# Performance work log

Measured on AMD Instinct MI355X. Metric: run time of the kernel, lower is better.

## Reference

```python
import jax, jax.numpy as jnp
import numpy as np

DIM_IN = 1024
DIM_OUT = 1024
NUM_HEADS = 16
HEAD_DIM = DIM_OUT // NUM_HEADS


def setup_inputs() -> dict:
    key = jax.random.key(0)
    k1, k2, k3, k4 = jax.random.split(key, 4)
    X = jax.random.normal(k1, (4, 2048, DIM_IN), dtype=jnp.float32)
    W_qkv = jax.random.normal(k2, (DIM_IN, 3 * DIM_OUT), dtype=jnp.float32) * (DIM_IN ** -0.5)
    W_out = jax.random.normal(k3, (DIM_OUT, DIM_OUT), dtype=jnp.float32) * (DIM_OUT ** -0.5)
    b_out = jax.random.normal(k4, (DIM_OUT,), dtype=jnp.float32) * 0.01
    return {"X": X, "W_qkv": W_qkv, "W_out": W_out, "b_out": b_out}


def reference(X, W_qkv, W_out, b_out):
    B, S, _ = X.shape
    qkv = X @ W_qkv  # [B, S, 3*dim_out]
    qkv = qkv.reshape(B, S, 3, NUM_HEADS, HEAD_DIM).transpose(2, 0, 3, 1, 4)
    q, k, v = qkv[0], qkv[1], qkv[2]  # each [B, H, S, hd]
    scores = jnp.einsum('bhqd,bhkd->bhqk', q, k)  # [B, H, S, S]
    causal = jnp.triu(jnp.ones((S, S), dtype=bool), k=1)
    scores = jnp.where(causal, -jnp.inf, scores)
    attn = jax.nn.softmax(scores * (HEAD_DIM ** -0.5), axis=-1)
    ctx = jnp.einsum('bhqk,bhkd->bhqd', attn, v)  # [B, H, S, hd]
    ctx = ctx.transpose(0, 2, 1, 3).reshape(B, S, DIM_OUT)
    return ctx @ W_out + b_out
```

## Files before the change

kernel.cpp:

```cpp
#include <hip/hip_runtime.h>
#include <hip/hip_bf16.h>

typedef __bf16 bf16_t;
typedef __bf16 bf16x8 __attribute__((ext_vector_type(8)));
typedef __bf16 bf16x4 __attribute__((ext_vector_type(4)));
typedef float f32x4 __attribute__((ext_vector_type(4)));
typedef float f32x16 __attribute__((ext_vector_type(16)));
typedef unsigned int u32x4 __attribute__((ext_vector_type(4)));

#define AS1(p) ((const __attribute__((address_space(1))) void*)(p))
#define AS3(p) ((__attribute__((address_space(3))) void*)(p))

#define QSCALE 0.1803368801111204f

__global__ void cast_x_kernel(const float* __restrict__ X, bf16_t* __restrict__ Xb) {
  int i = (blockIdx.x * 256 + threadIdx.x) * 4;
  float4 v = *(const float4*)(X + i);
  bf16x4 o;
  o[0] = (bf16_t)v.x; o[1] = (bf16_t)v.y; o[2] = (bf16_t)v.z; o[3] = (bf16_t)v.w;
  *(bf16x4*)(Xb + i) = o;
}

__global__ void transpose_cast_kernel(const float* __restrict__ W, bf16_t* __restrict__ Wt,
                                      int K, int N) {
  __shared__ float tile[32][33];
  int n0 = blockIdx.x * 32, k0 = blockIdx.y * 32;
  int tx = threadIdx.x, ty = threadIdx.y;
  for (int r = ty; r < 32; r += 8)
    tile[r][tx] = W[(size_t)(k0 + r) * N + n0 + tx];
  __syncthreads();
  for (int r = ty; r < 32; r += 8)
    Wt[(size_t)(n0 + r) * K + k0 + tx] = (bf16_t)tile[tx][r];
}

__global__ __launch_bounds__(256) void gemm_qkv_kernel(
    const bf16_t* __restrict__ A, const bf16_t* __restrict__ Bt,
    bf16_t* __restrict__ Qb, bf16_t* __restrict__ Kb, bf16_t* __restrict__ Vt) {
  __shared__ __align__(16) bf16_t As[128 * 32];
  __shared__ __align__(16) bf16_t Bs[128 * 32];
  const int tid = threadIdx.x;
  const int lane = tid & 63, wave = tid >> 6;
  const int quad = lane >> 4, l15 = lane & 15;
  const int wr = wave >> 1, wc = wave & 1;
  const int m0 = blockIdx.x * 128, n0 = blockIdx.y * 128;
  f32x4 acc[4][4];
  const f32x4 vzero = {0.f, 0.f, 0.f, 0.f};
#pragma unroll
  for (int i = 0; i < 4; i++)
#pragma unroll
    for (int j = 0; j < 4; j++) acc[i][j] = vzero;

  for (int kb = 0; kb < 1024; kb += 32) {
    __syncthreads();
#pragma unroll
    for (int i = 0; i < 2; i++) {
      int c = i * 256 + tid;
      int row = c >> 2, kc = c & 3;
      __builtin_amdgcn_global_load_lds(AS1(A + (size_t)(m0 + row) * 1024 + kb + kc * 8),
                                       AS3(As + c * 8), 16, 0, 0);
    }
#pragma unroll
    for (int i = 0; i < 2; i++) {
      int c = i * 256 + tid;
      int row = c >> 2, kc = c & 3;
      __builtin_amdgcn_global_load_lds(AS1(Bt + (size_t)(n0 + row) * 1024 + kb + kc * 8),
                                       AS3(Bs + c * 8), 16, 0, 0);
    }
    __builtin_amdgcn_s_waitcnt(0);
    __syncthreads();
    bf16x8 af[4], bfr[4];
#pragma unroll
    for (int t = 0; t < 4; t++) {
      af[t]  = *(const bf16x8*)(As + (wr * 64 + t * 16 + l15) * 32 + quad * 8);
      bfr[t] = *(const bf16x8*)(Bs + (wc * 64 + t * 16 + l15) * 32 + quad * 8);
    }
#pragma unroll
    for (int mt = 0; mt < 4; mt++)
#pragma unroll
      for (int nt = 0; nt < 4; nt++)
        acc[mt][nt] = __builtin_amdgcn_mfma_f32_16x16x32_bf16(af[mt], bfr[nt], acc[mt][nt], 0, 0, 0);
  }
#pragma unroll
  for (int nt = 0; nt < 4; nt++) {
    int gn = n0 + wc * 64 + nt * 16 + l15;
    int which = gn >> 10;
    int rem = gn & 1023;
    int hh = rem >> 6, dd = rem & 63;
    if (which == 2) {
#pragma unroll
      for (int mt = 0; mt < 4; mt++) {
        int gm0 = m0 + wr * 64 + mt * 16 + quad * 4;
        int b = gm0 >> 11, s = gm0 & 2047;
        bf16x4 o;
#pragma unroll
        for (int r = 0; r < 4; r++) o[r] = (bf16_t)acc[mt][nt][r];
        *(bf16x4*)(Vt + ((size_t)((b << 4) + hh) * 64 + dd) * 2048 + s) = o;
      }
    } else {
      bf16_t* dst = (which == 0) ? Qb : Kb;
      float scl = (which == 0) ? QSCALE : 1.0f;
#pragma unroll
      for (int mt = 0; mt < 4; mt++) {
#pragma unroll
        for (int r = 0; r < 4; r++) {
          int gm = m0 + wr * 64 + mt * 16 + quad * 4 + r;
          int b = gm >> 11, s = gm & 2047;
          dst[((size_t)((b << 4) + hh) * 2048 + s) * 64 + dd] = (bf16_t)(acc[mt][nt][r] * scl);
        }
      }
    }
  }
}

__device__ inline unsigned pack_bf16x2(float a, float b) {
  unsigned short lo = __builtin_bit_cast(unsigned short, (bf16_t)a);
  unsigned short hi = __builtin_bit_cast(unsigned short, (bf16_t)b);
  return (unsigned)lo | ((unsigned)hi << 16);
}

__global__ __launch_bounds__(256, 2) void attn_kernel(
    const bf16_t* __restrict__ Qg_, const bf16_t* __restrict__ Kg_,
    const bf16_t* __restrict__ Vtg_, bf16_t* __restrict__ ctx) {
  __shared__ __align__(16) bf16_t Ksm[2][128 * 64];
  __shared__ __align__(16) bf16_t Vsm[2][64 * 128];
  __shared__ float Lsh[128];
  const int tid = threadIdx.x;
  const int lane = tid & 63, w = tid >> 6;
  const int l31 = lane & 31, hl = lane >> 5;

  const int bh = blockIdx.x >> 3;
  const int pp = blockIdx.x & 7;
  const int b = bh >> 4, h = bh & 15;
  const size_t base = (size_t)bh * 2048 * 64;
  const bf16_t* Qg = Qg_ + base;
  const bf16_t* Kg = Kg_ + base;
  const bf16_t* Vtg = Vtg_ + base;

  auto stage_kv = [&](int bb, int jn) {
#pragma unroll
    for (int i = 0; i < 4; i++) {
      int slot = i * 256 + tid;
      int row = slot >> 3, c = (slot & 7) ^ (row & 7);
      __builtin_amdgcn_global_load_lds(AS1(Kg + ((size_t)jn * 128 + row) * 64 + c * 8),
                                       AS3(&Ksm[bb][0] + slot * 8), 16, 0, 0);
    }
#pragma unroll
    for (int i = 0; i < 4; i++) {
      int slot = i * 256 + tid;
      int d = slot >> 4, c = (slot & 15) ^ (d & 15);
      __builtin_amdgcn_global_load_lds(AS1(Vtg + (size_t)d * 2048 + jn * 128 + c * 8),
                                       AS3(&Vsm[bb][0] + slot * 8), 16, 0, 0);
    }
  };

  int cur = 0;
  stage_kv(0, 0);

  for (int ti = 0; ti < 2; ti++) {
    const int qb = (ti == 0) ? pp : 15 - pp;
    const int L = qb + 1;
    const int qg = qb * 128 + w * 32 + l31;

    bf16x8 aq[4];
#pragma unroll
    for (int kk = 0; kk < 4; kk++)
      aq[kk] = *(const bf16x8*)(Qg + (size_t)qg * 64 + kk * 16 + hl * 8);

    f32x16 Oacc[2];
#pragma unroll
    for (int nv = 0; nv < 2; nv++)
#pragma unroll
      for (int e = 0; e < 16; e++) Oacc[nv][e] = 0.f;
    float Lpart = 0.f;

    for (int j = 0; j < L; j++) {
      asm volatile("s_waitcnt vmcnt(0)" ::: "memory");
      __syncthreads();
      const bool havenext = (j + 1 < L) || (ti == 0);
      if (havenext) stage_kv(cur ^ 1, (j + 1 < L) ? j + 1 : 0);

      const bf16_t* Kb = &Ksm[cur][0];
      const bf16_t* Vb = &Vsm[cur][0];
      const bool diag = (j == qb);
      const int ntmax = diag ? (w + 1) : 4;

      for (int nt = 0; nt < ntmax; nt++) {
        f32x16 sc;
#pragma unroll
        for (int e = 0; e < 16; e++) sc[e] = 0.f;
        __builtin_amdgcn_s_setprio(1);
#pragma unroll
        for (int kk = 0; kk < 4; kk++) {
          bf16x8 ak = *(const bf16x8*)(Kb + ((nt * 32 + l31) * 8 + ((kk * 2 + hl) ^ (l31 & 7))) * 8);
          sc = __builtin_amdgcn_mfma_f32_32x32x16_bf16(ak, aq[kk], sc, 0, 0, 0);
        }
        __builtin_amdgcn_s_setprio(0);

        float p[16];
        const bool me = diag && (nt == w);
#pragma unroll
        for (int r = 0; r < 16; r++) {
          const int koff = (r & 3) + 8 * (r >> 2) + 4 * hl;
          p[r] = (me && (koff > l31)) ? 0.f : __builtin_exp2f(sc[r]);
        }
        {
          float a0 = p[0] + p[1], a1 = p[2] + p[3], a2 = p[4] + p[5], a3 = p[6] + p[7];
          float a4 = p[8] + p[9], a5 = p[10] + p[11], a6 = p[12] + p[13], a7 = p[14] + p[15];
          Lpart += ((a0 + a1) + (a2 + a3)) + ((a4 + a5) + (a6 + a7));
        }

        unsigned own0 = pack_bf16x2(p[0], p[1]),   own1 = pack_bf16x2(p[2], p[3]);
        unsigned own2 = pack_bf16x2(p[4], p[5]),   own3 = pack_bf16x2(p[6], p[7]);
        unsigned own4 = pack_bf16x2(p[8], p[9]),   own5 = pack_bf16x2(p[10], p[11]);
        unsigned own6 = pack_bf16x2(p[12], p[13]), own7 = pack_bf16x2(p[14], p[15]);
        unsigned r0 = __shfl_xor(hl ? own0 : own2, 32, 64);
        unsigned r1 = __shfl_xor(hl ? own1 : own3, 32, 64);
        unsigned r2 = __shfl_xor(hl ? own4 : own6, 32, 64);
        unsigned r3 = __shfl_xor(hl ? own5 : own7, 32, 64);
        u32x4 w0, w1;
        w0[0] = hl ? r0 : own0;  w0[1] = hl ? r1 : own1;
        w0[2] = hl ? own2 : r0;  w0[3] = hl ? own3 : r1;
        w1[0] = hl ? r2 : own4;  w1[1] = hl ? r3 : own5;
        w1[2] = hl ? own6 : r2;  w1[3] = hl ? own7 : r3;
        bf16x8 pa0 = __builtin_bit_cast(bf16x8, w0);
        bf16x8 pa1 = __builtin_bit_cast(bf16x8, w1);

        __builtin_amdgcn_s_setprio(1);
#pragma unroll
        for (int nv = 0; nv < 2; nv++) {
          const int dr = nv * 32 + l31;
          bf16x8 bv0 = *(const bf16x8*)(Vb + (dr * 16 + ((4 * nt + hl) ^ (dr & 15))) * 8);
          Oacc[nv] = __builtin_amdgcn_mfma_f32_32x32x16_bf16(pa0, bv0, Oacc[nv], 0, 0, 0);
          bf16x8 bv1 = *(const bf16x8*)(Vb + (dr * 16 + ((4 * nt + 2 + hl) ^ (dr & 15))) * 8);
          Oacc[nv] = __builtin_amdgcn_mfma_f32_32x32x16_bf16(pa1, bv1, Oacc[nv], 0, 0, 0);
        }
        __builtin_amdgcn_s_setprio(0);
      }
      cur ^= 1;
    }

    float Lf = Lpart + __shfl_xor(Lpart, 32, 64);
    if (hl == 0) Lsh[w * 32 + l31] = Lf;
#pragma unroll
    for (int r = 0; r < 16; r++) {
      const int crow = (r & 3) + 8 * (r >> 2) + 4 * hl;
      const float rl = __builtin_amdgcn_rcpf(Lsh[w * 32 + crow]);
      const int qrow = qb * 128 + w * 32 + crow;
#pragma unroll
      for (int nv = 0; nv < 2; nv++)
        ctx[((size_t)b * 2048 + qrow) * 1024 + h * 64 + nv * 32 + l31] =
            (bf16_t)(Oacc[nv][r] * rl);
    }
  }
}

__global__ __launch_bounds__(256) void gemm_out_kernel(
    const bf16_t* __restrict__ A, const bf16_t* __restrict__ Bt,
    const float* __restrict__ bias, float* __restrict__ out) {
  __shared__ __align__(16) bf16_t As[128 * 32];
  __shared__ __align__(16) bf16_t Bs[128 * 32];
  const int tid = threadIdx.x;
  const int lane = tid & 63, wave = tid >> 6;
  const int quad = lane >> 4, l15 = lane & 15;
  const int wr = wave >> 1, wc = wave & 1;
  const int m0 = blockIdx.x * 128, n0 = blockIdx.y * 128;
  f32x4 acc[4][4];
  const f32x4 vzero = {0.f, 0.f, 0.f, 0.f};
#pragma unroll
  for (int i = 0; i < 4; i++)
#pragma unroll
    for (int j = 0; j < 4; j++) acc[i][j] = vzero;

  for (int kb = 0; kb < 1024; kb += 32) {
    __syncthreads();
#pragma unroll
    for (int i = 0; i < 2; i++) {
      int c = i * 256 + tid;
      int row = c >> 2, kc = c & 3;
      __builtin_amdgcn_global_load_lds(AS1(A + (size_t)(m0 + row) * 1024 + kb + kc * 8),
                                       AS3(As + c * 8), 16, 0, 0);
    }
#pragma unroll
    for (int i = 0; i < 2; i++) {
      int c = i * 256 + tid;
      int row = c >> 2, kc = c & 3;
      __builtin_amdgcn_global_load_lds(AS1(Bt + (size_t)(n0 + row) * 1024 + kb + kc * 8),
                                       AS3(Bs + c * 8), 16, 0, 0);
    }
    __builtin_amdgcn_s_waitcnt(0);
    __syncthreads();
    bf16x8 af[4], bfr[4];
#pragma unroll
    for (int t = 0; t < 4; t++) {
      af[t]  = *(const bf16x8*)(As + (wr * 64 + t * 16 + l15) * 32 + quad * 8);
      bfr[t] = *(const bf16x8*)(Bs + (wc * 64 + t * 16 + l15) * 32 + quad * 8);
    }
#pragma unroll
    for (int mt = 0; mt < 4; mt++)
#pragma unroll
      for (int nt = 0; nt < 4; nt++)
        acc[mt][nt] = __builtin_amdgcn_mfma_f32_16x16x32_bf16(af[mt], bfr[nt], acc[mt][nt], 0, 0, 0);
  }
#pragma unroll
  for (int nt = 0; nt < 4; nt++) {
    int gn = n0 + wc * 64 + nt * 16 + l15;
    float bv = bias[gn];
#pragma unroll
    for (int mt = 0; mt < 4; mt++) {
#pragma unroll
      for (int r = 0; r < 4; r++) {
        int gm = m0 + wr * 64 + mt * 16 + quad * 4 + r;
        out[(size_t)gm * 1024 + gn] = acc[mt][nt][r] + bv;
      }
    }
  }
}

extern "C" void kernel_launch(void* const* d_in, const int* in_sizes, int n_in,
                              void* d_out, int out_size, void* d_ws, size_t ws_size,
                              hipStream_t stream) {
  (void)in_sizes; (void)n_in; (void)out_size; (void)ws_size;
  const float* X     = (const float*)d_in[0];
  const float* W_qkv = (const float*)d_in[1];
  const float* W_out = (const float*)d_in[2];
  const float* b_out = (const float*)d_in[3];
  float* out = (float*)d_out;

  char* ws = (char*)d_ws;
  bf16_t* Xb    = (bf16_t*)(ws);
  bf16_t* Wqkvt = (bf16_t*)(ws + 16777216);
  bf16_t* Woutt = (bf16_t*)(ws + 23068672);
  bf16_t* Qb    = (bf16_t*)(ws + 25165824);
  bf16_t* Kb    = (bf16_t*)(ws + 41943040);
  bf16_t* Vt    = (bf16_t*)(ws + 58720256);
  bf16_t* ctx   = (bf16_t*)(ws + 75497472);

  cast_x_kernel<<<8192, 256, 0, stream>>>(X, Xb);
  transpose_cast_kernel<<<dim3(96, 32), dim3(32, 8), 0, stream>>>(W_qkv, Wqkvt, 1024, 3072);
  transpose_cast_kernel<<<dim3(32, 32), dim3(32, 8), 0, stream>>>(W_out, Woutt, 1024, 1024);
  gemm_qkv_kernel<<<dim3(64, 24), 256, 0, stream>>>(Xb, Wqkvt, Qb, Kb, Vt);
  attn_kernel<<<dim3(512), 256, 0, stream>>>(Qb, Kb, Vt, ctx);
  gemm_out_kernel<<<dim3(64, 8), 256, 0, stream>>>(ctx, Woutt, b_out, out);
}
```

Baseline: 268.3 us.

## Permute K rows to drop P shuffles and compute row sums via MFMA

Reorders the K rows read for the score MFMA so that the resulting P accumulator layout already matches the A-operand layout of the PV MFMA. This removes the cross-half-wave shuffles and selects. The softmax denominator is now accumulated by extra MFMAs against a ones vector, which replaces the scalar adds, the shuffle and the shared-memory Lsh round trip. It also precomputes the LDS addresses and fully unrolls the nt loop with separate diagonal and off-diagonal paths. The cost is two extra MFMAs per tile and more registers for Lacc.

```diff
diff --git a/kernel.cpp b/kernel.cpp
--- a/kernel.cpp
+++ b/kernel.cpp
@@ -123,10 +123,10 @@
     const bf16_t* __restrict__ Vtg_, bf16_t* __restrict__ ctx) {
   __shared__ __align__(16) bf16_t Ksm[2][128 * 64];
   __shared__ __align__(16) bf16_t Vsm[2][64 * 128];
-  __shared__ float Lsh[128];
   const int tid = threadIdx.x;
   const int lane = tid & 63, w = tid >> 6;
   const int l31 = lane & 31, hl = lane >> 5;
+  const int krow = (l31 & 0x13) | ((l31 & 4) << 1) | ((l31 & 8) >> 1);
 
   const int bh = blockIdx.x >> 3;
   const int pp = blockIdx.x & 7;
@@ -136,6 +136,17 @@
   const bf16_t* Kg = Kg_ + base;
   const bf16_t* Vtg = Vtg_ + base;
 
+  int kadr[4];
+#pragma unroll
+  for (int kk = 0; kk < 4; kk++)
+    kadr[kk] = (krow * 8 + ((kk * 2 + hl) ^ (krow & 7))) * 8;
+  int vadr[2];
+#pragma unroll
+  for (int nv = 0; nv < 2; nv++) {
+    const int dr = nv * 32 + l31;
+    vadr[nv] = (dr * 16 + (hl ^ (dr & 15))) * 8;
+  }
+
   auto stage_kv = [&](int bb, int jn) {
 #pragma unroll
     for (int i = 0; i < 4; i++) {
@@ -153,6 +164,10 @@
     }
   };
 
+  bf16x8 bone;
+#pragma unroll
+  for (int e = 0; e < 8; e++) bone[e] = (bf16_t)1.0f;
+
   int cur = 0;
   stage_kv(0, 0);
 
@@ -166,12 +181,9 @@
     for (int kk = 0; kk < 4; kk++)
       aq[kk] = *(const bf16x8*)(Qg + (size_t)qg * 64 + kk * 16 + hl * 8);
 
-    f32x16 Oacc[2];
-#pragma unroll
-    for (int nv = 0; nv < 2; nv++)
-#pragma unroll
-      for (int e = 0; e < 16; e++) Oacc[nv][e] = 0.f;
-    float Lpart = 0.f;
+    f32x16 Oacc[2], Lacc;
+#pragma unroll
+    for (int e = 0; e < 16; e++) { Oacc[0][e] = 0.f; Oacc[1][e] = 0.f; Lacc[e] = 0.f; }
 
     for (int j = 0; j < L; j++) {
       asm volatile("s_waitcnt vmcnt(0)" ::: "memory");
@@ -182,69 +194,63 @@
       const bf16_t* Kb = &Ksm[cur][0];
       const bf16_t* Vb = &Vsm[cur][0];
       const bool diag = (j == qb);
-      const int ntmax = diag ? (w + 1) : 4;
-
-      for (int nt = 0; nt < ntmax; nt++) {
+
+      auto nt_body = [&](int nt, bool masked) {
         f32x16 sc;
 #pragma unroll
         for (int e = 0; e < 16; e++) sc[e] = 0.f;
         __builtin_amdgcn_s_setprio(1);
 #pragma unroll
         for (int kk = 0; kk < 4; kk++) {
-          bf16x8 ak = *(const bf16x8*)(Kb + ((nt * 32 + l31) * 8 + ((kk * 2 + hl) ^ (l31 & 7))) * 8);
+          bf16x8 ak = *(const bf16x8*)(Kb + nt * 2048 + kadr[kk]);
           sc = __builtin_amdgcn_mfma_f32_32x32x16_bf16(ak, aq[kk], sc, 0, 0, 0);
         }
         __builtin_amdgcn_s_setprio(0);
 
         float p[16];
-        const bool me = diag && (nt == w);
 #pragma unroll
         for (int r = 0; r < 16; r++) {
-          const int koff = (r & 3) + 8 * (r >> 2) + 4 * hl;
-          p[r] = (me && (koff > l31)) ? 0.f : __builtin_exp2f(sc[r]);
+          const int koff = hl * 8 + (r & 7) + 16 * (r >> 3);
+          float x = sc[r];
+          p[r] = (masked && (koff > l31)) ? 0.f : __builtin_exp2f(x);
         }
-        {
-          float a0 = p[0] + p[1], a1 = p[2] + p[3], a2 = p[4] + p[5], a3 = p[6] + p[7];
-          float a4 = p[8] + p[9], a5 = p[10] + p[11], a6 = p[12] + p[13], a7 = p[14] + p[15];
-          Lpart += ((a0 + a1) + (a2 + a3)) + ((a4 + a5) + (a6 + a7));
-        }
-
-        unsigned own0 = pack_bf16x2(p[0], p[1]),   own1 = pack_bf16x2(p[2], p[3]);
-        unsigned own2 = pack_bf16x2(p[4], p[5]),   own3 = pack_bf16x2(p[6], p[7]);
-        unsigned own4 = pack_bf16x2(p[8], p[9]),   own5 = pack_bf16x2(p[10], p[11]);
-        unsigned own6 = pack_bf16x2(p[12], p[13]), own7 = pack_bf16x2(p[14], p[15]);
-        unsigned r0 = __shfl_xor(hl ? own0 : own2, 32, 64);
-        unsigned r1 = __shfl_xor(hl ? own1 : own3, 32, 64);
-        unsigned r2 = __shfl_xor(hl ? own4 : own6, 32, 64);
-        unsigned r3 = __shfl_xor(hl ? own5 : own7, 32, 64);
+
         u32x4 w0, w1;
-        w0[0] = hl ? r0 : own0;  w0[1] = hl ? r1 : own1;
-        w0[2] = hl ? own2 : r0;  w0[3] = hl ? own3 : r1;
-        w1[0] = hl ? r2 : own4;  w1[1] = hl ? r3 : own5;
-        w1[2] = hl ? own6 : r2;  w1[3] = hl ? own7 : r3;
+        w0[0] = pack_bf16x2(p[0], p[1]);   w0[1] = pack_bf16x2(p[2], p[3]);
+        w0[2] = pack_bf16x2(p[4], p[5]);   w0[3] = pack_bf16x2(p[6], p[7]);
+        w1[0] = pack_bf16x2(p[8], p[9]);   w1[1] = pack_bf16x2(p[10], p[11]);
+        w1[2] = pack_bf16x2(p[12], p[13]); w1[3] = pack_bf16x2(p[14], p[15]);
         bf16x8 pa0 = __builtin_bit_cast(bf16x8, w0);
         bf16x8 pa1 = __builtin_bit_cast(bf16x8, w1);
 
         __builtin_amdgcn_s_setprio(1);
+        Lacc = __builtin_amdgcn_mfma_f32_32x32x16_bf16(pa0, bone, Lacc, 0, 0, 0);
+        Lacc = __builtin_amdgcn_mfma_f32_32x32x16_bf16(pa1, bone, Lacc, 0, 0, 0);
 #pragma unroll
         for (int nv = 0; nv < 2; nv++) {
-          const int dr = nv * 32 + l31;
-          bf16x8 bv0 = *(const bf16x8*)(Vb + (dr * 16 + ((4 * nt + hl) ^ (dr & 15))) * 8);
+          bf16x8 bv0 = *(const bf16x8*)(Vb + (vadr[nv] ^ ((4 * nt) * 8)));
           Oacc[nv] = __builtin_amdgcn_mfma_f32_32x32x16_bf16(pa0, bv0, Oacc[nv], 0, 0, 0);
-          bf16x8 bv1 = *(const bf16x8*)(Vb + (dr * 16 + ((4 * nt + 2 + hl) ^ (dr & 15))) * 8);
+          bf16x8 bv1 = *(const bf16x8*)(Vb + (vadr[nv] ^ ((4 * nt + 2) * 8)));
           Oacc[nv] = __builtin_amdgcn_mfma_f32_32x32x16_bf16(pa1, bv1, Oacc[nv], 0, 0, 0);
         }
         __builtin_amdgcn_s_setprio(0);
+      };
+
+      if (!diag) {
+#pragma unroll
+        for (int nt = 0; nt < 4; nt++) nt_body(nt, false);
+      } else {
+#pragma unroll
+        for (int nt = 0; nt < 4; nt++)
+          if (nt <= w) nt_body(nt, nt == w);
       }
       cur ^= 1;
     }
 
-    float Lf = Lpart + __shfl_xor(Lpart, 32, 64);
-    if (hl == 0) Lsh[w * 32 + l31] = Lf;
 #pragma unroll
     for (int r = 0; r < 16; r++) {
       const int crow = (r & 3) + 8 * (r >> 2) + 4 * hl;
-      const float rl = __builtin_amdgcn_rcpf(Lsh[w * 32 + crow]);
+      const float rl = __builtin_amdgcn_rcpf(Lacc[r]);
       const int qrow = qb * 128 + w * 32 + crow;
 #pragma unroll
       for (int nv = 0; nv < 2; nv++)
```

After: 264.1 us. Within noise of the previous version (-1.6%).
